# Kernel optimization log

Hardware: AMD Instinct MI355X
Metric: run time of the kernel (lower is better)

Reference implementation:

```python
import jax, jax.numpy as jnp
import numpy as np

N, R, K = 4, 16384, 96


def setup_inputs() -> dict:
    key = jax.random.key(0)
    k1, k2, k3 = jax.random.split(key, 3)
    rgbs = jax.random.uniform(k1, (N, R, K, 3), dtype=jnp.float32)
    sigmas = jax.random.normal(k2, (N, R, K, 1), dtype=jnp.float32)
    # depths must be monotonically increasing along K (ray sample depths in [0.5, 3.5])
    depths = jnp.sort(0.5 + 3.0 * jax.random.uniform(k3, (N, R, K, 1), dtype=jnp.float32), axis=2)
    return {"rgbs": rgbs, "sigmas": sigmas, "depths": depths}


def reference(rgbs, sigmas, depths):
    # Default rendering_options: use_max_depth=False, no_dist=False,
    # use_mid_point=True, clamp_mode='mipnerf', last_back=False,
    # normalize_rgb=False, normalize_depth=True, clip_depth=True, white_back=False.
    deltas = depths[:, :, 1:] - depths[:, :, :-1]                  # [N,R,K-1,1]
    # midpoint averaging
    rgbs_m = 0.5 * (rgbs[:, :, :-1] + rgbs[:, :, 1:])              # [N,R,K-1,3]
    sigmas_m = 0.5 * (sigmas[:, :, :-1] + sigmas[:, :, 1:])        # [N,R,K-1,1]
    depths_m = 0.5 * (depths[:, :, :-1] + depths[:, :, 1:])        # [N,R,K-1,1]
    # mipnerf clamp: softplus(sigma - 1)
    sig = jax.nn.softplus(sigmas_m - 1.0)
    alphas = 1.0 - jnp.exp(-deltas * sig)                          # [N,R,K-1,1]
    # transmittance via exclusive cumprod along the sample axis
    alphas_shifted = jnp.concatenate(
        [jnp.ones_like(alphas[:, :, :1]), 1.0 - alphas + 1e-10], axis=-2)
    trans = jnp.cumprod(alphas_shifted, axis=-2)[:, :, :-1]        # [N,R,K-1,1]
    weights = alphas * trans                                       # [N,R,K-1,1]
    weights_sum = weights.sum(axis=2)                              # [N,R,1]
    composite_rgb = jnp.sum(weights * rgbs_m, axis=-2)             # [N,R,3]
    composite_depth = jnp.sum(weights * depths_m, axis=-2)         # [N,R,1]
    # normalize_depth=True
    composite_depth = composite_depth / weights_sum
    # clip_depth=True
    composite_depth = jnp.nan_to_num(composite_depth, nan=jnp.inf)
    composite_depth = jnp.clip(composite_depth, depths_m.min(), depths_m.max())
    composite_rgb = composite_rgb * 2.0 - 1.0
    return composite_rgb, composite_depth, weights
```

## Files before the change

kernel.cpp:

```cpp
#include <hip/hip_runtime.h>
#include <math.h>

#define NRAYS     65536
#define KM1       95
#define RGB_OFF   0
#define DEPTH_OFF (NRAYS * 3)
#define W_OFF     (NRAYS * 4)

typedef float f4u __attribute__((ext_vector_type(4), aligned(4)));

__device__ __forceinline__ float one_minus_alpha(float x, float delta) {
    const float L2E = 1.44269504088896340736f;
    float xl = x * L2E;
    float l2 = (x > 20.0f) ? xl
                           : __builtin_amdgcn_logf(1.0f + __builtin_amdgcn_exp2f(xl));
    return __builtin_amdgcn_exp2f(-delta * l2);
}

__global__ __launch_bounds__(256) void integrate_kernel(
    const float* __restrict__ rgbs,
    const float* __restrict__ sigmas,
    const float* __restrict__ depths,
    float* __restrict__ out)
{
    const int t   = threadIdx.x;
    const int seg = t & 3;
    const int ray = blockIdx.x * 64 + (t >> 2);

    const float* db = depths + ray * 96  + seg * 24;
    const float* sb = sigmas + ray * 96  + seg * 24;
    const float* rb = rgbs   + ray * 288 + seg * 72;

    float u[24];
    float Tloc = 1.0f;
    float Sw = 0.f, Sd = 0.f, Sr = 0.f, Sg = 0.f, Sb = 0.f;
    float d0f=0.f, s0f=0.f, r0f=0.f, g0f=0.f, b0f=0.f, d1f=0.f, dpen=0.f;
    float dp=0.f, sp=0.f, rp=0.f, gp=0.f, bp=0.f;

#define DO_IV(IDX, dA,sA,rA,gA,bA, dB,sB,rB,gB,bB)                 \
    { float delta = (dB) - (dA);                                   \
      float x = 0.5f * ((sA) + (sB)) - 1.0f;                       \
      float e = one_minus_alpha(x, delta);                         \
      float uu = (1.0f - e) * Tloc;                                \
      Tloc *= e + 1e-10f;                                          \
      u[IDX] = uu;                                                 \
      Sw += uu;                                                    \
      Sd += uu * (0.5f * ((dA) + (dB)));                           \
      Sr += uu * (0.5f * ((rA) + (rB)));                           \
      Sg += uu * (0.5f * ((gA) + (gB)));                           \
      Sb += uu * (0.5f * ((bA) + (bB))); }

    #pragma unroll
    for (int j = 0; j < 6; ++j) {
        float4 d4 = *(const float4*)(db + 4*j);
        float4 s4 = *(const float4*)(sb + 4*j);
        float4 r0 = *(const float4*)(rb + 12*j);
        float4 r1 = *(const float4*)(rb + 12*j + 4);
        float4 r2 = *(const float4*)(rb + 12*j + 8);
        if (j == 0) {
            d0f=d4.x; s0f=s4.x; r0f=r0.x; g0f=r0.y; b0f=r0.z; d1f=d4.y;
        } else {
            DO_IV(4*j-1, dp,sp,rp,gp,bp, d4.x,s4.x,r0.x,r0.y,r0.z);
        }
        DO_IV(4*j+0, d4.x,s4.x,r0.x,r0.y,r0.z,  d4.y,s4.y,r0.w,r1.x,r1.y);
        DO_IV(4*j+1, d4.y,s4.y,r0.w,r1.x,r1.y,  d4.z,s4.z,r1.z,r1.w,r2.x);
        DO_IV(4*j+2, d4.z,s4.z,r1.z,r1.w,r2.x,  d4.w,s4.w,r2.y,r2.z,r2.w);
        if (j == 5) dpen = d4.z;
        dp=d4.w; sp=s4.w; rp=r2.y; gp=r2.z; bp=r2.w;
    }

    float dn = __shfl_down(d0f, 1);
    float sn = __shfl_down(s0f, 1);
    float rn = __shfl_down(r0f, 1);
    float gn = __shfl_down(g0f, 1);
    float bn = __shfl_down(b0f, 1);
    if (seg < 3) {
        DO_IV(23, dp,sp,rp,gp,bp, dn,sn,rn,gn,bn);
    } else {
        u[23] = 0.0f;
    }

    float incl = Tloc;
    float p1 = __shfl_up(incl, 1); if (seg >= 1) incl *= p1;
    float p2 = __shfl_up(incl, 2); if (seg >= 2) incl *= p2;
    float Tin = __shfl_up(incl, 1);
    if (seg == 0) Tin = 1.0f;

    Sw *= Tin; Sd *= Tin; Sr *= Tin; Sg *= Tin; Sb *= Tin;
    #pragma unroll
    for (int off = 1; off <= 2; off <<= 1) {
        Sw += __shfl_xor(Sw, off);
        Sd += __shfl_xor(Sd, off);
        Sr += __shfl_xor(Sr, off);
        Sg += __shfl_xor(Sg, off);
        Sb += __shfl_xor(Sb, off);
    }

    float* wout = out + W_OFF + ray * 95 + seg * 24;
    if (seg < 3) {
        #pragma unroll
        for (int k = 0; k < 6; ++k) {
            f4u v = { Tin*u[4*k], Tin*u[4*k+1], Tin*u[4*k+2], Tin*u[4*k+3] };
            *(f4u*)(wout + 4*k) = v;
        }
    } else {
        #pragma unroll
        for (int k = 0; k < 5; ++k) {
            f4u v = { Tin*u[4*k], Tin*u[4*k+1], Tin*u[4*k+2], Tin*u[4*k+3] };
            *(f4u*)(wout + 4*k) = v;
        }
        wout[20] = Tin*u[20];
        wout[21] = Tin*u[21];
        wout[22] = Tin*u[22];
    }

    float hiloc = 0.5f * (dpen + dp);
    const int lane = t & 63;
    float hi = __shfl(hiloc, lane | 3);
    if (seg == 0) {
        out[RGB_OFF + ray*3 + 0] = 2.f*Sr - 1.f;
        out[RGB_OFF + ray*3 + 1] = 2.f*Sg - 1.f;
        out[RGB_OFF + ray*3 + 2] = 2.f*Sb - 1.f;
        float dv = Sd / Sw;
        float lo = 0.5f * (d0f + d1f);
        dv = fmaxf(fminf(dv, hi), lo);
        out[DEPTH_OFF + ray] = dv;
    }
#undef DO_IV
}

extern "C" void kernel_launch(void* const* d_in, const int* in_sizes, int n_in,
                              void* d_out, int out_size, void* d_ws, size_t ws_size,
                              hipStream_t stream) {
    const float* rgbs   = (const float*)d_in[0];
    const float* sigmas = (const float*)d_in[1];
    const float* depths = (const float*)d_in[2];
    float* out = (float*)d_out;

    integrate_kernel<<<NRAYS / 64, 256, 0, stream>>>(rgbs, sigmas, depths, out);
}
```

Baseline: 177.8 us.

## Split each ray across 16 lanes with overlapping loads and DPP scans

Each ray is now processed by 16 lanes, each handling 6 intervals, instead of 4 lanes handling 24. Each lane loads one overlapping sample rather than exchanging boundary values through shuffles. The transmittance prefix product and the sum reductions use DPP row_shr/row_bcast operations instead of ds_bpermute-based shuffles. The aim is more memory-level parallelism, lower register pressure and cheaper cross-lane communication. The cost is smaller float2 loads, some redundant boundary loads, and misaligned 16-byte weight stores.

```diff
diff --git a/kernel.cpp b/kernel.cpp
--- a/kernel.cpp
+++ b/kernel.cpp
@@ -2,12 +2,16 @@
 #include <math.h>
 
 #define NRAYS     65536
-#define KM1       95
 #define RGB_OFF   0
 #define DEPTH_OFF (NRAYS * 3)
 #define W_OFF     (NRAYS * 4)
 
 typedef float f4u __attribute__((ext_vector_type(4), aligned(4)));
+typedef float f2u __attribute__((ext_vector_type(2), aligned(4)));
+
+#define DPPF(oldv, x, ctrl)                                                    \
+    __int_as_float(__builtin_amdgcn_update_dpp(                                \
+        __float_as_int(oldv), __float_as_int(x), (ctrl), 0xF, 0xF, false))
 
 __device__ __forceinline__ float one_minus_alpha(float x, float delta) {
     const float L2E = 1.44269504088896340736f;
@@ -23,110 +27,101 @@
     const float* __restrict__ depths,
     float* __restrict__ out)
 {
-    const int t   = threadIdx.x;
-    const int seg = t & 3;
-    const int ray = blockIdx.x * 64 + (t >> 2);
+    const int t    = threadIdx.x;
+    const int l    = t & 15;
+    const int ray  = blockIdx.x * 16 + (t >> 4);
+    const bool full = (l < 15);
 
-    const float* db = depths + ray * 96  + seg * 24;
-    const float* sb = sigmas + ray * 96  + seg * 24;
-    const float* rb = rgbs   + ray * 288 + seg * 72;
+    const float* db = depths + ray * 96  + 6 * l;
+    const float* sb = sigmas + ray * 96  + 6 * l;
+    const float* rb = rgbs   + ray * 288 + 18 * l;
 
-    float u[24];
+    float2 e0 = *(const float2*)(db);
+    float2 e1 = *(const float2*)(db + 2);
+    float2 e2 = *(const float2*)(db + 4);
+    float  d6 = full ? db[6] : 0.f;
+    float2 f0 = *(const float2*)(sb);
+    float2 f1 = *(const float2*)(sb + 2);
+    float2 f2v = *(const float2*)(sb + 4);
+    float  s6 = full ? sb[6] : 0.f;
+    float2 c0 = *(const float2*)(rb);
+    float2 c1 = *(const float2*)(rb + 2);
+    float2 c2 = *(const float2*)(rb + 4);
+    float2 c3 = *(const float2*)(rb + 6);
+    float2 c4 = *(const float2*)(rb + 8);
+    float2 c5 = *(const float2*)(rb + 10);
+    float2 c6 = *(const float2*)(rb + 12);
+    float2 c7 = *(const float2*)(rb + 14);
+    float2 c8 = *(const float2*)(rb + 16);
+    float2 c9 = full ? *(const float2*)(rb + 18) : float2{0.f, 0.f};
+    float  r20 = full ? rb[20] : 0.f;
+
+    const float D[7] = {e0.x, e0.y, e1.x, e1.y, e2.x, e2.y, d6};
+    const float S[7] = {f0.x, f0.y, f1.x, f1.y, f2v.x, f2v.y, s6};
+    const float R[7] = {c0.x, c1.y, c3.x, c4.y, c6.x, c7.y, c9.x};
+    const float G[7] = {c0.y, c2.x, c3.y, c5.x, c6.y, c8.x, c9.y};
+    const float B[7] = {c1.x, c2.y, c4.x, c5.y, c7.x, c8.y, r20};
+
+    float u[6];
     float Tloc = 1.0f;
-    float Sw = 0.f, Sd = 0.f, Sr = 0.f, Sg = 0.f, Sb = 0.f;
-    float d0f=0.f, s0f=0.f, r0f=0.f, g0f=0.f, b0f=0.f, d1f=0.f, dpen=0.f;
-    float dp=0.f, sp=0.f, rp=0.f, gp=0.f, bp=0.f;
+    float Sw = 0.f, Sd = 0.f, Sr = 0.f, Sg = 0.f, Sbv = 0.f;
 
-#define DO_IV(IDX, dA,sA,rA,gA,bA, dB,sB,rB,gB,bB)                 \
-    { float delta = (dB) - (dA);                                   \
-      float x = 0.5f * ((sA) + (sB)) - 1.0f;                       \
-      float e = one_minus_alpha(x, delta);                         \
-      float uu = (1.0f - e) * Tloc;                                \
-      Tloc *= e + 1e-10f;                                          \
-      u[IDX] = uu;                                                 \
-      Sw += uu;                                                    \
-      Sd += uu * (0.5f * ((dA) + (dB)));                           \
-      Sr += uu * (0.5f * ((rA) + (rB)));                           \
-      Sg += uu * (0.5f * ((gA) + (gB)));                           \
-      Sb += uu * (0.5f * ((bA) + (bB))); }
+#define DO_IV(I)                                                      \
+    { float delta = D[(I)+1] - D[I];                                  \
+      float x = 0.5f * (S[I] + S[(I)+1]) - 1.0f;                      \
+      float e = one_minus_alpha(x, delta);                            \
+      float uu = (1.0f - e) * Tloc;                                   \
+      Tloc *= e + 1e-10f;                                             \
+      u[I] = uu;                                                      \
+      Sw  += uu;                                                      \
+      Sd  += uu * (0.5f * (D[I] + D[(I)+1]));                         \
+      Sr  += uu * (0.5f * (R[I] + R[(I)+1]));                         \
+      Sg  += uu * (0.5f * (G[I] + G[(I)+1]));                         \
+      Sbv += uu * (0.5f * (B[I] + B[(I)+1])); }
 
-    #pragma unroll
-    for (int j = 0; j < 6; ++j) {
-        float4 d4 = *(const float4*)(db + 4*j);
-        float4 s4 = *(const float4*)(sb + 4*j);
-        float4 r0 = *(const float4*)(rb + 12*j);
-        float4 r1 = *(const float4*)(rb + 12*j + 4);
-        float4 r2 = *(const float4*)(rb + 12*j + 8);
-        if (j == 0) {
-            d0f=d4.x; s0f=s4.x; r0f=r0.x; g0f=r0.y; b0f=r0.z; d1f=d4.y;
-        } else {
-            DO_IV(4*j-1, dp,sp,rp,gp,bp, d4.x,s4.x,r0.x,r0.y,r0.z);
-        }
-        DO_IV(4*j+0, d4.x,s4.x,r0.x,r0.y,r0.z,  d4.y,s4.y,r0.w,r1.x,r1.y);
-        DO_IV(4*j+1, d4.y,s4.y,r0.w,r1.x,r1.y,  d4.z,s4.z,r1.z,r1.w,r2.x);
-        DO_IV(4*j+2, d4.z,s4.z,r1.z,r1.w,r2.x,  d4.w,s4.w,r2.y,r2.z,r2.w);
-        if (j == 5) dpen = d4.z;
-        dp=d4.w; sp=s4.w; rp=r2.y; gp=r2.z; bp=r2.w;
+    DO_IV(0) DO_IV(1) DO_IV(2) DO_IV(3) DO_IV(4)
+    if (full) { DO_IV(5) } else { u[5] = 0.f; }
+#undef DO_IV
+
+    float incl = Tloc;
+    incl *= DPPF(1.0f, incl, 0x111);
+    incl *= DPPF(1.0f, incl, 0x112);
+    incl *= DPPF(1.0f, incl, 0x114);
+    incl *= DPPF(1.0f, incl, 0x118);
+    float Tin = DPPF(1.0f, incl, 0x111);
+
+    Sw *= Tin; Sd *= Tin; Sr *= Tin; Sg *= Tin; Sbv *= Tin;
+
+#define RED(v)                         \
+    v += DPPF(0.f, v, 0x111);          \
+    v += DPPF(0.f, v, 0x112);          \
+    v += DPPF(0.f, v, 0x114);          \
+    v += DPPF(0.f, v, 0x118);
+    RED(Sw) RED(Sd) RED(Sr) RED(Sg) RED(Sbv)
+#undef RED
+
+    float lo0 = 0.5f * (D[0] + D[1]);
+    float lo  = DPPF(0.f, lo0, 0x11F);
+
+    float* wout = out + W_OFF + ray * 95 + 6 * l;
+    f4u v4 = { Tin * u[0], Tin * u[1], Tin * u[2], Tin * u[3] };
+    *(f4u*)wout = v4;
+    if (full) {
+        f2u v2 = { Tin * u[4], Tin * u[5] };
+        *(f2u*)(wout + 4) = v2;
+    } else {
+        wout[4] = Tin * u[4];
     }
 
-    float dn = __shfl_down(d0f, 1);
-    float sn = __shfl_down(s0f, 1);
-    float rn = __shfl_down(r0f, 1);
-    float gn = __shfl_down(g0f, 1);
-    float bn = __shfl_down(b0f, 1);
-    if (seg < 3) {
-        DO_IV(23, dp,sp,rp,gp,bp, dn,sn,rn,gn,bn);
-    } else {
-        u[23] = 0.0f;
-    }
-
-    float incl = Tloc;
-    float p1 = __shfl_up(incl, 1); if (seg >= 1) incl *= p1;
-    float p2 = __shfl_up(incl, 2); if (seg >= 2) incl *= p2;
-    float Tin = __shfl_up(incl, 1);
-    if (seg == 0) Tin = 1.0f;
-
-    Sw *= Tin; Sd *= Tin; Sr *= Tin; Sg *= Tin; Sb *= Tin;
-    #pragma unroll
-    for (int off = 1; off <= 2; off <<= 1) {
-        Sw += __shfl_xor(Sw, off);
-        Sd += __shfl_xor(Sd, off);
-        Sr += __shfl_xor(Sr, off);
-        Sg += __shfl_xor(Sg, off);
-        Sb += __shfl_xor(Sb, off);
-    }
-
-    float* wout = out + W_OFF + ray * 95 + seg * 24;
-    if (seg < 3) {
-        #pragma unroll
-        for (int k = 0; k < 6; ++k) {
-            f4u v = { Tin*u[4*k], Tin*u[4*k+1], Tin*u[4*k+2], Tin*u[4*k+3] };
-            *(f4u*)(wout + 4*k) = v;
-        }
-    } else {
-        #pragma unroll
-        for (int k = 0; k < 5; ++k) {
-            f4u v = { Tin*u[4*k], Tin*u[4*k+1], Tin*u[4*k+2], Tin*u[4*k+3] };
-            *(f4u*)(wout + 4*k) = v;
-        }
-        wout[20] = Tin*u[20];
-        wout[21] = Tin*u[21];
-        wout[22] = Tin*u[22];
-    }
-
-    float hiloc = 0.5f * (dpen + dp);
-    const int lane = t & 63;
-    float hi = __shfl(hiloc, lane | 3);
-    if (seg == 0) {
-        out[RGB_OFF + ray*3 + 0] = 2.f*Sr - 1.f;
-        out[RGB_OFF + ray*3 + 1] = 2.f*Sg - 1.f;
-        out[RGB_OFF + ray*3 + 2] = 2.f*Sb - 1.f;
+    if (l == 15) {
+        out[RGB_OFF + ray * 3 + 0] = 2.f * Sr  - 1.f;
+        out[RGB_OFF + ray * 3 + 1] = 2.f * Sg  - 1.f;
+        out[RGB_OFF + ray * 3 + 2] = 2.f * Sbv - 1.f;
         float dv = Sd / Sw;
-        float lo = 0.5f * (d0f + d1f);
+        float hi = 0.5f * (D[4] + D[5]);
         dv = fmaxf(fminf(dv, hi), lo);
         out[DEPTH_OFF + ray] = dv;
     }
-#undef DO_IV
 }
 
 extern "C" void kernel_launch(void* const* d_in, const int* in_sizes, int n_in,
@@ -137,5 +132,5 @@
     const float* depths = (const float*)d_in[2];
     float* out = (float*)d_out;
 
-    integrate_kernel<<<NRAYS / 64, 256, 0, stream>>>(rgbs, sigmas, depths, out);
+    integrate_kernel<<<NRAYS / 16, 256, 0, stream>>>(rgbs, sigmas, depths, out);
 }
```

New measurement: 157.6 us. 1.13x faster.
